# Performance work log

Measured on AMD Instinct MI355X. Metric: run time of the kernel, lower is better.

The kernel has to match this reference:

```python
import jax, jax.numpy as jnp
import numpy as np

N_SRC, N_DST, E = 10000, 10000, 640000
S, T, O, H = 128, 128, 128, 4
D = O // H


def setup_inputs() -> dict:
    key = jax.random.key(0)
    ks = jax.random.split(key, 12)
    f = lambda k, shape, fan: jax.random.normal(k, shape, dtype=jnp.float32) / np.float32(np.sqrt(fan))
    return {
        "x_src": jax.random.normal(ks[0], (N_SRC, S), dtype=jnp.float32),
        "x_dst": jax.random.normal(ks[1], (N_DST, T), dtype=jnp.float32),
        "W_pred1": f(ks[2], (S, T), T),
        "b_pred1": jnp.zeros((S,), jnp.float32),
        "W_pred2": f(ks[3], (S, S), S),
        "b_pred2": jnp.zeros((S,), jnp.float32),
        "W_res": f(ks[4], (H * D, S), S),
        "W_src": f(ks[5], (H * D, S), S),
        "W_dst": f(ks[6], (H * D, T), T),
        "att_src": jax.random.normal(ks[7], (1, H, D), dtype=jnp.float32) * 0.01,
        "att_dst": jax.random.normal(ks[8], (1, H, D), dtype=jnp.float32) * 0.01,
        "W_self": f(ks[9], (H * D, T), T),
        "b_self": jnp.zeros((H * D,), jnp.float32),
        "edge_src": jax.random.randint(ks[10], (E,), 0, N_SRC),
        "edge_dst": jax.random.randint(ks[11], (E,), 0, N_DST),
        "num_dst": N_DST,
    }


def reference(x_src, x_dst, W_pred1, b_pred1, W_pred2, b_pred2, W_res, W_src, W_dst,
              att_src, att_dst, W_self, b_self, edge_src, edge_dst, num_dst):
    h, d = att_src.shape[1], att_src.shape[2]
    # residual prediction path: pred_mlp(x_dst) = Lin2(ReLU(Lin1(x_dst)))
    pred = jax.nn.relu(x_dst @ W_pred1.T + b_pred1) @ W_pred2.T + b_pred2  # [Ndst,S]
    residual = x_src[edge_src] - pred[edge_dst]                            # [E,S]
    # per-node attention logits (equivalent to gather-then-dot, cheaper)
    a_s = ((x_src @ W_src.T).reshape(-1, h, d) * att_src).sum(-1)          # [Nsrc,H]
    a_d = ((x_dst @ W_dst.T).reshape(-1, h, d) * att_dst).sum(-1)          # [Ndst,H]
    alpha = jax.nn.leaky_relu(a_s[edge_src] + a_d[edge_dst], 0.2)          # [E,H]
    # edge softmax over incoming edges of each destination node
    amax = jax.ops.segment_max(alpha, edge_dst, num_segments=num_dst)      # [Ndst,H]
    ex = jnp.exp(alpha - amax[edge_dst])
    denom = jax.ops.segment_sum(ex, edge_dst, num_segments=num_dst)
    alpha = ex / (denom[edge_dst] + 1e-16)                                 # [E,H]
    # attention-weighted aggregation of transformed residuals
    msg = (residual @ W_res.T).reshape(-1, h, d) * alpha[:, :, None]       # [E,H,D]
    agg = jax.ops.segment_sum(msg.reshape(-1, h * d), edge_dst, num_segments=num_dst)
    return agg + x_dst @ W_self.T + b_self                                 # [Ndst,H*D]
```

## Files before the change

kernel.cpp:

```cpp
#include <hip/hip_runtime.h>

#define LEAKY 0.2f
#define CAP 160
#define CAPB 8192
#define CHUNK 2048
#define GSTRIDE 32

#define FMA4(A, S, V) do { (A).x += (S)*(V).x; (A).y += (S)*(V).y; (A).z += (S)*(V).z; (A).w += (S)*(V).w; } while (0)

struct GemmJob { const float* X; const float* W; const float* B; float* Y; int M; int relu; int bf16out; };

__device__ __forceinline__ unsigned short f2bf(float f) {
  unsigned int u = __float_as_uint(f);
  u += 0x7FFFu + ((u >> 16) & 1u);
  return (unsigned short)(u >> 16);
}
__device__ __forceinline__ float bf2f(unsigned short h) {
  return __uint_as_float(((unsigned int)h) << 16);
}

__device__ __forceinline__ void gemm128_block(
    const float* __restrict__ X, const float* __restrict__ W,
    const float* __restrict__ B, float* __restrict__ Y,
    int M, int relu, int bf16out, int row0,
    float* __restrict__ XsT , float* __restrict__ WTs ) {
  if (row0 >= M) return;
  const int tid = threadIdx.x;
  const int tx = tid & 15;
  const int ty = tid >> 4;
  float4 acc[8][2];
#pragma unroll
  for (int i = 0; i < 8; i++) {
    acc[i][0] = make_float4(0.f, 0.f, 0.f, 0.f);
    acc[i][1] = make_float4(0.f, 0.f, 0.f, 0.f);
  }
  const int rS = tid >> 1;
  const int kb = (tid & 1) * 8;

  for (int k0 = 0; k0 < 128; k0 += 16) {
    int rr = row0 + rS; if (rr >= M) rr = M - 1;
    const float* xp = X + (size_t)rr * 128 + k0 + kb;
    float4 a0 = *(const float4*)xp;
    float4 a1 = *(const float4*)(xp + 4);
    XsT[(kb + 0) * 128 + rS] = a0.x; XsT[(kb + 1) * 128 + rS] = a0.y;
    XsT[(kb + 2) * 128 + rS] = a0.z; XsT[(kb + 3) * 128 + rS] = a0.w;
    XsT[(kb + 4) * 128 + rS] = a1.x; XsT[(kb + 5) * 128 + rS] = a1.y;
    XsT[(kb + 6) * 128 + rS] = a1.z; XsT[(kb + 7) * 128 + rS] = a1.w;

    const float* wp = W + (size_t)rS * 128 + k0 + kb;
    float4 b0 = *(const float4*)wp;
    float4 b1 = *(const float4*)(wp + 4);
    WTs[(kb + 0) * 128 + rS] = b0.x; WTs[(kb + 1) * 128 + rS] = b0.y;
    WTs[(kb + 2) * 128 + rS] = b0.z; WTs[(kb + 3) * 128 + rS] = b0.w;
    WTs[(kb + 4) * 128 + rS] = b1.x; WTs[(kb + 5) * 128 + rS] = b1.y;
    WTs[(kb + 6) * 128 + rS] = b1.z; WTs[(kb + 7) * 128 + rS] = b1.w;
    __syncthreads();

#pragma unroll
    for (int k = 0; k < 16; k++) {
      float4 xa = *(const float4*)&XsT[k * 128 + ty * 4];
      float4 xb = *(const float4*)&XsT[k * 128 + 64 + ty * 4];
      float4 w0 = *(const float4*)&WTs[k * 128 + tx * 4];
      float4 w1 = *(const float4*)&WTs[k * 128 + 64 + tx * 4];
      FMA4(acc[0][0], xa.x, w0); FMA4(acc[0][1], xa.x, w1);
      FMA4(acc[1][0], xa.y, w0); FMA4(acc[1][1], xa.y, w1);
      FMA4(acc[2][0], xa.z, w0); FMA4(acc[2][1], xa.z, w1);
      FMA4(acc[3][0], xa.w, w0); FMA4(acc[3][1], xa.w, w1);
      FMA4(acc[4][0], xb.x, w0); FMA4(acc[4][1], xb.x, w1);
      FMA4(acc[5][0], xb.y, w0); FMA4(acc[5][1], xb.y, w1);
      FMA4(acc[6][0], xb.z, w0); FMA4(acc[6][1], xb.z, w1);
      FMA4(acc[7][0], xb.w, w0); FMA4(acc[7][1], xb.w, w1);
    }
    __syncthreads();
  }

  float4 bv0 = make_float4(0.f, 0.f, 0.f, 0.f);
  float4 bv1 = make_float4(0.f, 0.f, 0.f, 0.f);
  if (B) { bv0 = *(const float4*)(B + tx * 4); bv1 = *(const float4*)(B + 64 + tx * 4); }
#pragma unroll
  for (int i = 0; i < 8; i++) {
    int r = row0 + (i < 4 ? ty * 4 + i : 64 + ty * 4 + (i - 4));
    if (r < M) {
      float4 o0, o1;
      o0.x = acc[i][0].x + bv0.x; o0.y = acc[i][0].y + bv0.y;
      o0.z = acc[i][0].z + bv0.z; o0.w = acc[i][0].w + bv0.w;
      o1.x = acc[i][1].x + bv1.x; o1.y = acc[i][1].y + bv1.y;
      o1.z = acc[i][1].z + bv1.z; o1.w = acc[i][1].w + bv1.w;
      if (relu) {
        o0.x = fmaxf(o0.x, 0.f); o0.y = fmaxf(o0.y, 0.f);
        o0.z = fmaxf(o0.z, 0.f); o0.w = fmaxf(o0.w, 0.f);
        o1.x = fmaxf(o1.x, 0.f); o1.y = fmaxf(o1.y, 0.f);
        o1.z = fmaxf(o1.z, 0.f); o1.w = fmaxf(o1.w, 0.f);
      }
      if (bf16out) {
        unsigned short* yb = (unsigned short*)Y;
        ushort4 p0, p1;
        p0.x = f2bf(o0.x); p0.y = f2bf(o0.y); p0.z = f2bf(o0.z); p0.w = f2bf(o0.w);
        p1.x = f2bf(o1.x); p1.y = f2bf(o1.y); p1.z = f2bf(o1.z); p1.w = f2bf(o1.w);
        *(ushort4*)(yb + (size_t)r * 128 + tx * 4) = p0;
        *(ushort4*)(yb + (size_t)r * 128 + 64 + tx * 4) = p1;
      } else {
        *(float4*)(Y + (size_t)r * 128 + tx * 4) = o0;
        *(float4*)(Y + (size_t)r * 128 + 64 + tx * 4) = o1;
      }
    }
  }
}

__device__ __forceinline__ void attn32_block(const float* __restrict__ X,
                                             const float* __restrict__ v,
                                             float* __restrict__ a, int M, int blk,
                                             float* __restrict__ vsf ) {
  int tid = threadIdx.x;
  for (int i = tid; i < 512; i += 256) vsf[i + ((i >> 5) << 2)] = v[i];
  __syncthreads();
  int g = tid >> 3, l = tid & 7;
  int n = blk * 32 + g;
  if (n >= M) return;
  const float* xp = X + (size_t)n * 128 + l * 16;
  float4 x0 = *(const float4*)xp;
  float4 x1 = *(const float4*)(xp + 4);
  float4 x2 = *(const float4*)(xp + 8);
  float4 x3 = *(const float4*)(xp + 12);
  const float4* vv = (const float4*)vsf;
  int s = l * 18;
  float4 p = make_float4(0.f, 0.f, 0.f, 0.f);
  FMA4(p, x0.x, vv[s + 0]); FMA4(p, x0.y, vv[s + 1]); FMA4(p, x0.z, vv[s + 2]); FMA4(p, x0.w, vv[s + 3]);
  FMA4(p, x1.x, vv[s + 4]); FMA4(p, x1.y, vv[s + 5]); FMA4(p, x1.z, vv[s + 6]); FMA4(p, x1.w, vv[s + 7]);
  FMA4(p, x2.x, vv[s + 9]); FMA4(p, x2.y, vv[s +10]); FMA4(p, x2.z, vv[s +11]); FMA4(p, x2.w, vv[s +12]);
  FMA4(p, x3.x, vv[s +13]); FMA4(p, x3.y, vv[s +14]); FMA4(p, x3.z, vv[s +15]); FMA4(p, x3.w, vv[s +16]);
#pragma unroll
  for (int off = 1; off < 8; off <<= 1) {
    p.x += __shfl_xor(p.x, off, 64);
    p.y += __shfl_xor(p.y, off, 64);
    p.z += __shfl_xor(p.z, off, 64);
    p.w += __shfl_xor(p.w, off, 64);
  }
  if (l == 0) *(float4*)(a + (size_t)n * 4) = p;
}

__global__ __launch_bounds__(256) void phase1(
    const float* __restrict__ Wsrc, const float* __restrict__ attsrc,
    const float* __restrict__ Wdst, const float* __restrict__ attdst,
    const float* __restrict__ W_res, const float* __restrict__ W2,
    const float* __restrict__ b2,
    GemmJob jA,
    float* __restrict__ v_src, float* __restrict__ v_dst,
    float* __restrict__ Wc, float* __restrict__ bc,
    const int* __restrict__ edge_src, const int* __restrict__ edge_dst,
    int* __restrict__ gcnt, int* __restrict__ bin,
    int E, int Nd, int NB, int GA, int Q1, int T1) {
  __shared__ float smem[4096];
  int bx = blockIdx.x, tid = threadIdx.x;
  int u = (bx & 7) * Q1 + (bx >> 3);
  if (u >= T1) return;
  if (u == 0) {
    int which = tid >> 7, k = tid & 127;
    const float* W = which ? Wdst : Wsrc;
    const float* att = which ? attdst : attsrc;
    float* v = which ? v_dst : v_src;
    float s[4] = {0.f, 0.f, 0.f, 0.f};
#pragma unroll
    for (int h = 0; h < 4; h++)
      for (int d = 0; d < 32; d++)
        s[h] += W[(size_t)(h * 32 + d) * 128 + k] * att[h * 32 + d];
#pragma unroll
    for (int h = 0; h < 4; h++) v[k * 4 + h] = s[h];
  } else if (u == 1) {
    if (tid < 128) {
      float s = 0.f;
      for (int i = 0; i < 128; i++) s += W_res[(size_t)tid * 128 + i] * b2[i];
      bc[tid] = s;
    }
  } else if (u < 66) {
    int id = (u - 2) * 256 + tid;
    int o = id >> 7, j = id & 127;
    float s = 0.f;
    for (int i = 0; i < 128; i++) s += W_res[(size_t)o * 128 + i] * W2[(size_t)i * 128 + j];
    Wc[(size_t)o * 128 + j] = s;
  } else if (u < 66 + GA) {
    gemm128_block(jA.X, jA.W, jA.B, jA.Y, jA.M, jA.relu, jA.bf16out,
                  (u - 66) * 128, smem, smem + 2048);
  } else {
    int* pk    = (int*)smem;
    int* hist  = (int*)smem + CHUNK;
    int* gbase = hist + 160;
    int* lcur  = gbase + 160;
    int e0 = (u - 66 - GA) * CHUNK;
    int n = E - e0; if (n > CHUNK) n = CHUNK;
    if (n <= 0) return;
    for (int i = tid; i < NB; i += 256) hist[i] = 0;
    __syncthreads();
    for (int i = tid; i < n; i += 256) {
      int s = edge_src[e0 + i], d = edge_dst[e0 + i];
      pk[i] = (s << 14) | d;
      atomicAdd(&hist[d >> 6], 1);
    }
    __syncthreads();
    for (int b = tid; b < NB; b += 256) {
      gbase[b] = hist[b] ? atomicAdd(&gcnt[b * GSTRIDE], hist[b]) : 0;
      lcur[b] = 0;
    }
    __syncthreads();
    for (int i = tid; i < n; i += 256) {
      int p = pk[i];
      int b = (p & 16383) >> 6;
      int off = gbase[b] + atomicAdd(&lcur[b], 1);
      if (off < CAPB) bin[(size_t)b * CAPB + off] = p;
    }
  }
}

__global__ __launch_bounds__(256) void phase2(
    GemmJob j0, GemmJob j1, GemmJob j2,
    const float* __restrict__ x_src, const float* __restrict__ x_dst,
    const float* __restrict__ v_src, const float* __restrict__ v_dst,
    float* __restrict__ a_s, float* __restrict__ a_d,
    const int* __restrict__ gcnt, const int* __restrict__ bin,
    int* __restrict__ sorted_src, int* __restrict__ rstart, int* __restrict__ rend,
    int Ns, int Nd, int NB, int G, int As, int Ad, int Q2, int T2) {
  __shared__ float smem[4096];
  int bx = blockIdx.x, tid = threadIdx.x;
  int u = (bx % 6) * Q2 + bx / 6;
  if (u >= T2) return;
  if (u < 3 * G) {
    GemmJob J = (u < G) ? j0 : (u < 2 * G) ? j1 : j2;
    gemm128_block(J.X, J.W, J.B, J.Y, J.M, J.relu, J.bf16out, (u % G) * 128, smem, smem + 2048);
  } else if (u < 3 * G + As) {
    attn32_block(x_src, v_src, a_s, Ns, u - 3 * G, smem);
  } else if (u < 3 * G + As + Ad) {
    attn32_block(x_dst, v_dst, a_d, Nd, u - 3 * G - As, smem);
  } else {
    int b = u - (3 * G + As + Ad);
    int* hist2 = (int*)smem;
    int* lcur2 = (int*)smem + 64;
    int cnt = gcnt[b * GSTRIDE]; if (cnt > CAPB) cnt = CAPB;
    size_t base = (size_t)b * CAPB;
    if (tid < 64) hist2[tid] = 0;
    __syncthreads();
    for (int i = tid; i < cnt; i += 256) atomicAdd(&hist2[bin[base + i] & 63], 1);
    __syncthreads();
    if (tid < 64) {
      int v = hist2[tid];
      int incl = v;
#pragma unroll
      for (int off = 1; off < 64; off <<= 1) {
        int t = __shfl_up(incl, off, 64);
        if (tid >= off) incl += t;
      }
      int st = incl - v;
      lcur2[tid] = st;
      int dst = (b << 6) + tid;
      if (dst < Nd) {
        rstart[dst] = (int)base + st;
        rend[dst]   = (int)base + st + v;
      }
    }
    __syncthreads();
    for (int i = tid; i < cnt; i += 256) {
      int p = bin[base + i];
      int j = p & 63;
      int lp = atomicAdd(&lcur2[j], 1);
      sorted_src[base + lp] = p >> 14;
    }
  }
}

__global__ __launch_bounds__(256) void phase3(
    const int* __restrict__ rstart, const int* __restrict__ rend,
    const int* __restrict__ sorted_src,
    const float* __restrict__ a_s, const float* __restrict__ a_d,
    const unsigned short* __restrict__ u_src, const float* __restrict__ u_pred,
    const float* __restrict__ self_o, float* __restrict__ out, int Nd) {
  __shared__ float smem[1920];
  int bx = blockIdx.x, tid = threadIdx.x;
  int half = tid >> 7;
  int t = tid & 127;
  int dst = bx * 2 + half;
  if (dst >= Nd) return;

  float* wbuf  = smem + half * 640;
  int* srcbuf  = (int*)(smem + 1280) + half * 160;
  float4* red4 = (float4*)(smem + 1600);
  float4* redv = (float4*)(smem + 1616) + half * 32;
  float* inv_s = smem + 1872 + half * 4;
  float* sA_s  = smem + 1880 + half * 4;

  int start = rstart[dst];
  int deg = rend[dst] - start;
  float4 ad4 = *(const float4*)(a_d + (size_t)dst * 4);
  float s0 = 0.f, s1 = 0.f, s2 = 0.f, s3 = 0.f;
  for (int i = t; i < deg; i += 128) {
    int src = sorted_src[start + i];
    float4 as4 = *(const float4*)(a_s + (size_t)src * 4);
    float l0 = as4.x + ad4.x; l0 = l0 > 0.f ? l0 : LEAKY * l0;
    float l1 = as4.y + ad4.y; l1 = l1 > 0.f ? l1 : LEAKY * l1;
    float l2 = as4.z + ad4.z; l2 = l2 > 0.f ? l2 : LEAKY * l2;
    float l3 = as4.w + ad4.w; l3 = l3 > 0.f ? l3 : LEAKY * l3;
    float w0 = __expf(l0), w1 = __expf(l1), w2 = __expf(l2), w3 = __expf(l3);
    if (i < CAP) {
      wbuf[i * 4 + 0] = w0; wbuf[i * 4 + 1] = w1;
      wbuf[i * 4 + 2] = w2; wbuf[i * 4 + 3] = w3;
      srcbuf[i] = src;
    }
    s0 += w0; s1 += w1; s2 += w2; s3 += w3;
  }
  int wave = tid >> 6;
#pragma unroll
  for (int off = 32; off > 0; off >>= 1) {
    s0 += __shfl_xor(s0, off, 64);
    s1 += __shfl_xor(s1, off, 64);
    s2 += __shfl_xor(s2, off, 64);
    s3 += __shfl_xor(s3, off, 64);
  }
  if ((tid & 63) == 0) red4[wave] = make_float4(s0, s1, s2, s3);
  __syncthreads();
  if (t == 0) {
    float4 A = red4[half * 2], B = red4[half * 2 + 1];
    float dx = A.x + B.x, dy = A.y + B.y, dz = A.z + B.z, dw = A.w + B.w;
    inv_s[0] = 1.f / (dx + 1e-16f); sA_s[0] = dx * inv_s[0];
    inv_s[1] = 1.f / (dy + 1e-16f); sA_s[1] = dy * inv_s[1];
    inv_s[2] = 1.f / (dz + 1e-16f); sA_s[2] = dz * inv_s[2];
    inv_s[3] = 1.f / (dw + 1e-16f); sA_s[3] = dw * inv_s[3];
  }
  __syncthreads();

  int c4 = t & 31, rgrp = t >> 5, h = c4 >> 3;
  int coff = c4 * 4;
  float4 acc0 = make_float4(0.f,0.f,0.f,0.f), acc1 = acc0, acc2 = acc0, acc3 = acc0;
  int cap = deg < CAP ? deg : CAP;
  int i = rgrp;
  for (; i + 12 < cap; i += 16) {
    int sA = srcbuf[i], sB = srcbuf[i + 4], sC = srcbuf[i + 8], sD = srcbuf[i + 12];
    float wA = wbuf[i * 4 + h], wB = wbuf[(i + 4) * 4 + h];
    float wC = wbuf[(i + 8) * 4 + h], wD = wbuf[(i + 12) * 4 + h];
    ushort4 hA = *(const ushort4*)(u_src + (size_t)sA * 128 + coff);
    ushort4 hB = *(const ushort4*)(u_src + (size_t)sB * 128 + coff);
    ushort4 hC = *(const ushort4*)(u_src + (size_t)sC * 128 + coff);
    ushort4 hD = *(const ushort4*)(u_src + (size_t)sD * 128 + coff);
    float4 uA = make_float4(bf2f(hA.x), bf2f(hA.y), bf2f(hA.z), bf2f(hA.w));
    float4 uB = make_float4(bf2f(hB.x), bf2f(hB.y), bf2f(hB.z), bf2f(hB.w));
    float4 uC = make_float4(bf2f(hC.x), bf2f(hC.y), bf2f(hC.z), bf2f(hC.w));
    float4 uD = make_float4(bf2f(hD.x), bf2f(hD.y), bf2f(hD.z), bf2f(hD.w));
    FMA4(acc0, wA, uA); FMA4(acc1, wB, uB); FMA4(acc2, wC, uC); FMA4(acc3, wD, uD);
  }
  for (; i < cap; i += 4) {
    int s_ = srcbuf[i];
    float w = wbuf[i * 4 + h];
    ushort4 hh = *(const ushort4*)(u_src + (size_t)s_ * 128 + coff);
    float4 uu = make_float4(bf2f(hh.x), bf2f(hh.y), bf2f(hh.z), bf2f(hh.w));
    FMA4(acc0, w, uu);
  }
  if (deg > CAP) {
    float adh = (h == 0) ? ad4.x : (h == 1) ? ad4.y : (h == 2) ? ad4.z : ad4.w;
    for (int k = CAP + rgrp; k < deg; k += 4) {
      int src = sorted_src[start + k];
      float l = a_s[(size_t)src * 4 + h] + adh;
      l = l > 0.f ? l : LEAKY * l;
      float w = __expf(l);
      ushort4 hh = *(const ushort4*)(u_src + (size_t)src * 128 + coff);
      float4 uu = make_float4(bf2f(hh.x), bf2f(hh.y), bf2f(hh.z), bf2f(hh.w));
      FMA4(acc0, w, uu);
    }
  }
  float4 acc;
  acc.x = acc0.x + acc1.x + acc2.x + acc3.x;
  acc.y = acc0.y + acc1.y + acc2.y + acc3.y;
  acc.z = acc0.z + acc1.z + acc2.z + acc3.z;
  acc.w = acc0.w + acc1.w + acc2.w + acc3.w;
  acc.x += __shfl_xor(acc.x, 32, 64);
  acc.y += __shfl_xor(acc.y, 32, 64);
  acc.z += __shfl_xor(acc.z, 32, 64);
  acc.w += __shfl_xor(acc.w, 32, 64);
  if (t >= 64 && t < 96) redv[c4] = acc;
  __syncthreads();
  if (t < 32) {
    float4 r = redv[c4];
    acc.x += r.x; acc.y += r.y; acc.z += r.z; acc.w += r.w;
    float4 up = *(const float4*)(u_pred + (size_t)dst * 128 + coff);
    float4 so = *(const float4*)(self_o + (size_t)dst * 128 + coff);
    float iv = inv_s[h], sa = sA_s[h];
    float4 o;
    o.x = acc.x * iv - sa * up.x + so.x;
    o.y = acc.y * iv - sa * up.y + so.y;
    o.z = acc.z * iv - sa * up.z + so.z;
    o.w = acc.w * iv - sa * up.w + so.w;
    *(float4*)(out + (size_t)dst * 128 + coff) = o;
  }
}

extern "C" void kernel_launch(void* const* d_in, const int* in_sizes, int n_in,
                              void* d_out, int out_size, void* d_ws, size_t ws_size,
                              hipStream_t stream) {
  const float* x_src   = (const float*)d_in[0];
  const float* x_dst   = (const float*)d_in[1];
  const float* W_pred1 = (const float*)d_in[2];
  const float* b_pred1 = (const float*)d_in[3];
  const float* W_pred2 = (const float*)d_in[4];
  const float* b_pred2 = (const float*)d_in[5];
  const float* W_res   = (const float*)d_in[6];
  const float* W_src   = (const float*)d_in[7];
  const float* W_dst   = (const float*)d_in[8];
  const float* att_src = (const float*)d_in[9];
  const float* att_dst = (const float*)d_in[10];
  const float* W_self  = (const float*)d_in[11];
  const float* b_self  = (const float*)d_in[12];
  const int* edge_src  = (const int*)d_in[13];
  const int* edge_dst  = (const int*)d_in[14];
  int Ns = in_sizes[0] / 128;
  int Nd = in_sizes[1] / 128;
  int E  = in_sizes[13];
  float* out = (float*)d_out;
  int NB = (Nd + 63) >> 6;

  char* ws = (char*)d_ws;
  auto alloc = [&](size_t bytes) -> char* {
    char* p = ws;
    ws += (bytes + 255) & ~(size_t)255;
    return p;
  };
  float* relu1  = (float*)alloc((size_t)Nd * 128 * 4);
  unsigned short* u_src = (unsigned short*)alloc((size_t)Ns * 128 * 2);
  float* u_pred = (float*)alloc((size_t)Nd * 128 * 4);
  float* self_o = (float*)alloc((size_t)Nd * 128 * 4);
  float* a_s    = (float*)alloc((size_t)Ns * 4 * 4);
  float* a_d    = (float*)alloc((size_t)Nd * 4 * 4);
  float* v_src  = (float*)alloc(128 * 4 * 4);
  float* v_dst  = (float*)alloc(128 * 4 * 4);
  float* Wc     = (float*)alloc(128 * 128 * 4);
  float* bc     = (float*)alloc(128 * 4);
  int* gcnt     = (int*)alloc((size_t)NB * GSTRIDE * 4);
  int* rstart   = (int*)alloc((size_t)Nd * 4);
  int* rend     = (int*)alloc((size_t)Nd * 4);
  int* bin      = (int*)alloc((size_t)NB * CAPB * 4);
  int* sorted_src = (int*)alloc((size_t)NB * CAPB * 4);

  hipMemsetAsync(gcnt, 0, (size_t)NB * GSTRIDE * sizeof(int), stream);

  int GA  = (Nd + 127) / 128;
  int NCH = (E + CHUNK - 1) / CHUNK;
  int T1 = 66 + GA + NCH;
  int Q1 = (T1 + 7) / 8;
  GemmJob jA{ x_dst, W_pred1, b_pred1, relu1, Nd, 1, 0 };
  hipLaunchKernelGGL(phase1, dim3(Q1 * 8), dim3(256), 0, stream,
                     W_src, att_src, W_dst, att_dst, W_res, W_pred2, b_pred2, jA,
                     v_src, v_dst, Wc, bc, edge_src, edge_dst, gcnt, bin,
                     E, Nd, NB, GA, Q1, T1);

  int maxM = Ns > Nd ? Ns : Nd;
  int G  = (maxM + 127) / 128;
  int As = (Ns + 31) / 32;
  int Ad = (Nd + 31) / 32;
  int T2 = 3 * G + As + Ad + NB;
  int Q2 = (T2 + 5) / 6;
  GemmJob jB{ x_src, W_res,  nullptr, (float*)u_src, Ns, 0, 1 };
  GemmJob jC{ x_dst, W_self, b_self,  self_o, Nd, 0, 0 };
  GemmJob jU{ relu1, Wc,     bc,      u_pred, Nd, 0, 0 };
  hipLaunchKernelGGL(phase2, dim3(Q2 * 6), dim3(256), 0, stream,
                     jB, jC, jU, x_src, x_dst, v_src, v_dst, a_s, a_d,
                     gcnt, bin, sorted_src, rstart, rend,
                     Ns, Nd, NB, G, As, Ad, Q2, T2);

  hipLaunchKernelGGL(phase3, dim3((Nd + 1) / 2), dim3(256), 0, stream,
                     rstart, rend, sorted_src, a_s, a_d, u_src, u_pred, self_o, out, Nd);
}
```

Baseline: 166.5 us.

## Rebalance phases and fuse softmax denominator into single-pass aggregation

```diff
diff --git a/kernel.cpp b/kernel.cpp
--- a/kernel.cpp
+++ b/kernel.cpp
@@ -1,7 +1,6 @@
 #include <hip/hip_runtime.h>
 
 #define LEAKY 0.2f
-#define CAP 160
 #define CAPB 8192
 #define CHUNK 2048
 #define GSTRIDE 32
@@ -107,12 +106,24 @@
   }
 }
 
-__device__ __forceinline__ void attn32_block(const float* __restrict__ X,
-                                             const float* __restrict__ v,
-                                             float* __restrict__ a, int M, int blk,
-                                             float* __restrict__ vsf ) {
+__device__ __forceinline__ void attn32v_block(const float* __restrict__ X,
+                                              const float* __restrict__ W,
+                                              const float* __restrict__ att,
+                                              float* __restrict__ a, int M, int blk,
+                                              float* __restrict__ vsf ) {
   int tid = threadIdx.x;
-  for (int i = tid; i < 512; i += 256) vsf[i + ((i >> 5) << 2)] = v[i];
+  {
+    int k = tid & 127, hh = tid >> 7;
+#pragma unroll
+    for (int p = 0; p < 2; p++) {
+      int h = hh + p * 2;
+      float s = 0.f;
+      for (int d = 0; d < 32; d++)
+        s += W[(size_t)(h * 32 + d) * 128 + k] * att[h * 32 + d];
+      int i = k * 4 + h;
+      vsf[i + ((i >> 5) << 2)] = s;
+    }
+  }
   __syncthreads();
   int g = tid >> 3, l = tid & 7;
   int n = blk * 32 + g;
@@ -144,49 +155,60 @@
     const float* __restrict__ Wdst, const float* __restrict__ attdst,
     const float* __restrict__ W_res, const float* __restrict__ W2,
     const float* __restrict__ b2,
-    GemmJob jA,
-    float* __restrict__ v_src, float* __restrict__ v_dst,
+    GemmJob jA, GemmJob jB, GemmJob jC,
+    const float* __restrict__ x_src, const float* __restrict__ x_dst,
+    float* __restrict__ a_s, float* __restrict__ a_d,
     float* __restrict__ Wc, float* __restrict__ bc,
     const int* __restrict__ edge_src, const int* __restrict__ edge_dst,
     int* __restrict__ gcnt, int* __restrict__ bin,
-    int E, int Nd, int NB, int GA, int Q1, int T1) {
+    int E, int Ns, int Nd, int NB,
+    int GA, int GB, int GC, int As, int Ad, int Q1, int T1) {
   __shared__ float smem[4096];
   int bx = blockIdx.x, tid = threadIdx.x;
   int u = (bx & 7) * Q1 + (bx >> 3);
   if (u >= T1) return;
   if (u == 0) {
-    int which = tid >> 7, k = tid & 127;
-    const float* W = which ? Wdst : Wsrc;
-    const float* att = which ? attdst : attsrc;
-    float* v = which ? v_dst : v_src;
-    float s[4] = {0.f, 0.f, 0.f, 0.f};
-#pragma unroll
-    for (int h = 0; h < 4; h++)
-      for (int d = 0; d < 32; d++)
-        s[h] += W[(size_t)(h * 32 + d) * 128 + k] * att[h * 32 + d];
-#pragma unroll
-    for (int h = 0; h < 4; h++) v[k * 4 + h] = s[h];
-  } else if (u == 1) {
     if (tid < 128) {
       float s = 0.f;
       for (int i = 0; i < 128; i++) s += W_res[(size_t)tid * 128 + i] * b2[i];
       bc[tid] = s;
     }
-  } else if (u < 66) {
-    int id = (u - 2) * 256 + tid;
+    return;
+  }
+  if (u < 65) {
+    int id = (u - 1) * 256 + tid;
     int o = id >> 7, j = id & 127;
     float s = 0.f;
     for (int i = 0; i < 128; i++) s += W_res[(size_t)o * 128 + i] * W2[(size_t)i * 128 + j];
     Wc[(size_t)o * 128 + j] = s;
-  } else if (u < 66 + GA) {
-    gemm128_block(jA.X, jA.W, jA.B, jA.Y, jA.M, jA.relu, jA.bf16out,
-                  (u - 66) * 128, smem, smem + 2048);
-  } else {
+    return;
+  }
+  int r = u - 65;
+  if (r < GA) {
+    gemm128_block(jA.X, jA.W, jA.B, jA.Y, jA.M, jA.relu, jA.bf16out, r * 128, smem, smem + 2048);
+    return;
+  }
+  r -= GA;
+  if (r < GB) {
+    gemm128_block(jB.X, jB.W, jB.B, jB.Y, jB.M, jB.relu, jB.bf16out, r * 128, smem, smem + 2048);
+    return;
+  }
+  r -= GB;
+  if (r < GC) {
+    gemm128_block(jC.X, jC.W, jC.B, jC.Y, jC.M, jC.relu, jC.bf16out, r * 128, smem, smem + 2048);
+    return;
+  }
+  r -= GC;
+  if (r < As) { attn32v_block(x_src, Wsrc, attsrc, a_s, Ns, r, smem); return; }
+  r -= As;
+  if (r < Ad) { attn32v_block(x_dst, Wdst, attdst, a_d, Nd, r, smem); return; }
+  r -= Ad;
+  {
     int* pk    = (int*)smem;
     int* hist  = (int*)smem + CHUNK;
     int* gbase = hist + 160;
     int* lcur  = gbase + 160;
-    int e0 = (u - 66 - GA) * CHUNK;
+    int e0 = r * CHUNK;
     int n = E - e0; if (n > CHUNK) n = CHUNK;
     if (n <= 0) return;
     for (int i = tid; i < NB; i += 256) hist[i] = 0;
@@ -212,57 +234,49 @@
 }
 
 __global__ __launch_bounds__(256) void phase2(
-    GemmJob j0, GemmJob j1, GemmJob j2,
-    const float* __restrict__ x_src, const float* __restrict__ x_dst,
-    const float* __restrict__ v_src, const float* __restrict__ v_dst,
-    float* __restrict__ a_s, float* __restrict__ a_d,
+    GemmJob jU,
     const int* __restrict__ gcnt, const int* __restrict__ bin,
     int* __restrict__ sorted_src, int* __restrict__ rstart, int* __restrict__ rend,
-    int Ns, int Nd, int NB, int G, int As, int Ad, int Q2, int T2) {
+    int Nd, int NB, int GU, int Q2, int T2) {
   __shared__ float smem[4096];
   int bx = blockIdx.x, tid = threadIdx.x;
-  int u = (bx % 6) * Q2 + bx / 6;
+  int u = (bx % 3) * Q2 + bx / 3;
   if (u >= T2) return;
-  if (u < 3 * G) {
-    GemmJob J = (u < G) ? j0 : (u < 2 * G) ? j1 : j2;
-    gemm128_block(J.X, J.W, J.B, J.Y, J.M, J.relu, J.bf16out, (u % G) * 128, smem, smem + 2048);
-  } else if (u < 3 * G + As) {
-    attn32_block(x_src, v_src, a_s, Ns, u - 3 * G, smem);
-  } else if (u < 3 * G + As + Ad) {
-    attn32_block(x_dst, v_dst, a_d, Nd, u - 3 * G - As, smem);
-  } else {
-    int b = u - (3 * G + As + Ad);
-    int* hist2 = (int*)smem;
-    int* lcur2 = (int*)smem + 64;
-    int cnt = gcnt[b * GSTRIDE]; if (cnt > CAPB) cnt = CAPB;
-    size_t base = (size_t)b * CAPB;
-    if (tid < 64) hist2[tid] = 0;
-    __syncthreads();
-    for (int i = tid; i < cnt; i += 256) atomicAdd(&hist2[bin[base + i] & 63], 1);
-    __syncthreads();
-    if (tid < 64) {
-      int v = hist2[tid];
-      int incl = v;
-#pragma unroll
-      for (int off = 1; off < 64; off <<= 1) {
-        int t = __shfl_up(incl, off, 64);
-        if (tid >= off) incl += t;
-      }
-      int st = incl - v;
-      lcur2[tid] = st;
-      int dst = (b << 6) + tid;
-      if (dst < Nd) {
-        rstart[dst] = (int)base + st;
-        rend[dst]   = (int)base + st + v;
-      }
-    }
-    __syncthreads();
-    for (int i = tid; i < cnt; i += 256) {
-      int p = bin[base + i];
-      int j = p & 63;
-      int lp = atomicAdd(&lcur2[j], 1);
-      sorted_src[base + lp] = p >> 14;
-    }
+  if (u < GU) {
+    gemm128_block(jU.X, jU.W, jU.B, jU.Y, jU.M, jU.relu, jU.bf16out, u * 128, smem, smem + 2048);
+    return;
+  }
+  int b = u - GU;
+  int* hist2 = (int*)smem;
+  int* lcur2 = (int*)smem + 64;
+  int cnt = gcnt[b * GSTRIDE]; if (cnt > CAPB) cnt = CAPB;
+  size_t base = (size_t)b * CAPB;
+  if (tid < 64) hist2[tid] = 0;
+  __syncthreads();
+  for (int i = tid; i < cnt; i += 256) atomicAdd(&hist2[bin[base + i] & 63], 1);
+  __syncthreads();
+  if (tid < 64) {
+    int v = hist2[tid];
+    int incl = v;
+#pragma unroll
+    for (int off = 1; off < 64; off <<= 1) {
+      int t = __shfl_up(incl, off, 64);
+      if (tid >= off) incl += t;
+    }
+    int st = incl - v;
+    lcur2[tid] = st;
+    int dst = (b << 6) + tid;
+    if (dst < Nd) {
+      rstart[dst] = (int)base + st;
+      rend[dst]   = (int)base + st + v;
+    }
+  }
+  __syncthreads();
+  for (int i = tid; i < cnt; i += 256) {
+    int p = bin[base + i];
+    int j = p & 63;
+    int lp = atomicAdd(&lcur2[j], 1);
+    sorted_src[base + lp] = p >> 14;
   }
 }
 
@@ -272,119 +286,76 @@
     const float* __restrict__ a_s, const float* __restrict__ a_d,
     const unsigned short* __restrict__ u_src, const float* __restrict__ u_pred,
     const float* __restrict__ self_o, float* __restrict__ out, int Nd) {
-  __shared__ float smem[1920];
+  __shared__ float4 redv[64];
+  __shared__ float  rdn[64];
   int bx = blockIdx.x, tid = threadIdx.x;
-  int half = tid >> 7;
-  int t = tid & 127;
+  int half = tid >> 7, t = tid & 127;
   int dst = bx * 2 + half;
   if (dst >= Nd) return;
-
-  float* wbuf  = smem + half * 640;
-  int* srcbuf  = (int*)(smem + 1280) + half * 160;
-  float4* red4 = (float4*)(smem + 1600);
-  float4* redv = (float4*)(smem + 1616) + half * 32;
-  float* inv_s = smem + 1872 + half * 4;
-  float* sA_s  = smem + 1880 + half * 4;
-
   int start = rstart[dst];
   int deg = rend[dst] - start;
-  float4 ad4 = *(const float4*)(a_d + (size_t)dst * 4);
-  float s0 = 0.f, s1 = 0.f, s2 = 0.f, s3 = 0.f;
-  for (int i = t; i < deg; i += 128) {
-    int src = sorted_src[start + i];
-    float4 as4 = *(const float4*)(a_s + (size_t)src * 4);
-    float l0 = as4.x + ad4.x; l0 = l0 > 0.f ? l0 : LEAKY * l0;
-    float l1 = as4.y + ad4.y; l1 = l1 > 0.f ? l1 : LEAKY * l1;
-    float l2 = as4.z + ad4.z; l2 = l2 > 0.f ? l2 : LEAKY * l2;
-    float l3 = as4.w + ad4.w; l3 = l3 > 0.f ? l3 : LEAKY * l3;
-    float w0 = __expf(l0), w1 = __expf(l1), w2 = __expf(l2), w3 = __expf(l3);
-    if (i < CAP) {
-      wbuf[i * 4 + 0] = w0; wbuf[i * 4 + 1] = w1;
-      wbuf[i * 4 + 2] = w2; wbuf[i * 4 + 3] = w3;
-      srcbuf[i] = src;
-    }
-    s0 += w0; s1 += w1; s2 += w2; s3 += w3;
-  }
-  int wave = tid >> 6;
-#pragma unroll
-  for (int off = 32; off > 0; off >>= 1) {
-    s0 += __shfl_xor(s0, off, 64);
-    s1 += __shfl_xor(s1, off, 64);
-    s2 += __shfl_xor(s2, off, 64);
-    s3 += __shfl_xor(s3, off, 64);
-  }
-  if ((tid & 63) == 0) red4[wave] = make_float4(s0, s1, s2, s3);
-  __syncthreads();
-  if (t == 0) {
-    float4 A = red4[half * 2], B = red4[half * 2 + 1];
-    float dx = A.x + B.x, dy = A.y + B.y, dz = A.z + B.z, dw = A.w + B.w;
-    inv_s[0] = 1.f / (dx + 1e-16f); sA_s[0] = dx * inv_s[0];
-    inv_s[1] = 1.f / (dy + 1e-16f); sA_s[1] = dy * inv_s[1];
-    inv_s[2] = 1.f / (dz + 1e-16f); sA_s[2] = dz * inv_s[2];
-    inv_s[3] = 1.f / (dw + 1e-16f); sA_s[3] = dw * inv_s[3];
-  }
-  __syncthreads();
-
-  int c4 = t & 31, rgrp = t >> 5, h = c4 >> 3;
-  int coff = c4 * 4;
-  float4 acc0 = make_float4(0.f,0.f,0.f,0.f), acc1 = acc0, acc2 = acc0, acc3 = acc0;
-  int cap = deg < CAP ? deg : CAP;
+  int c4 = t & 31, rgrp = t >> 5, h = c4 >> 3, coff = c4 * 4;
+  float adh = a_d[(size_t)dst * 4 + h];
+
+  float4 acc[8];
+  float dnm[4] = {0.f, 0.f, 0.f, 0.f};
+#pragma unroll
+  for (int j = 0; j < 8; j++) acc[j] = make_float4(0.f, 0.f, 0.f, 0.f);
+
   int i = rgrp;
-  for (; i + 12 < cap; i += 16) {
-    int sA = srcbuf[i], sB = srcbuf[i + 4], sC = srcbuf[i + 8], sD = srcbuf[i + 12];
-    float wA = wbuf[i * 4 + h], wB = wbuf[(i + 4) * 4 + h];
-    float wC = wbuf[(i + 8) * 4 + h], wD = wbuf[(i + 12) * 4 + h];
-    ushort4 hA = *(const ushort4*)(u_src + (size_t)sA * 128 + coff);
-    ushort4 hB = *(const ushort4*)(u_src + (size_t)sB * 128 + coff);
-    ushort4 hC = *(const ushort4*)(u_src + (size_t)sC * 128 + coff);
-    ushort4 hD = *(const ushort4*)(u_src + (size_t)sD * 128 + coff);
-    float4 uA = make_float4(bf2f(hA.x), bf2f(hA.y), bf2f(hA.z), bf2f(hA.w));
-    float4 uB = make_float4(bf2f(hB.x), bf2f(hB.y), bf2f(hB.z), bf2f(hB.w));
-    float4 uC = make_float4(bf2f(hC.x), bf2f(hC.y), bf2f(hC.z), bf2f(hC.w));
-    float4 uD = make_float4(bf2f(hD.x), bf2f(hD.y), bf2f(hD.z), bf2f(hD.w));
-    FMA4(acc0, wA, uA); FMA4(acc1, wB, uB); FMA4(acc2, wC, uC); FMA4(acc3, wD, uD);
-  }
-  for (; i < cap; i += 4) {
-    int s_ = srcbuf[i];
-    float w = wbuf[i * 4 + h];
-    ushort4 hh = *(const ushort4*)(u_src + (size_t)s_ * 128 + coff);
-    float4 uu = make_float4(bf2f(hh.x), bf2f(hh.y), bf2f(hh.z), bf2f(hh.w));
-    FMA4(acc0, w, uu);
-  }
-  if (deg > CAP) {
-    float adh = (h == 0) ? ad4.x : (h == 1) ? ad4.y : (h == 2) ? ad4.z : ad4.w;
-    for (int k = CAP + rgrp; k < deg; k += 4) {
-      int src = sorted_src[start + k];
+  for (; i + 28 < deg; i += 32) {
+#pragma unroll
+    for (int j = 0; j < 8; j++) {
+      int src = sorted_src[start + i + j * 4];
       float l = a_s[(size_t)src * 4 + h] + adh;
       l = l > 0.f ? l : LEAKY * l;
       float w = __expf(l);
-      ushort4 hh = *(const ushort4*)(u_src + (size_t)src * 128 + coff);
-      float4 uu = make_float4(bf2f(hh.x), bf2f(hh.y), bf2f(hh.z), bf2f(hh.w));
-      FMA4(acc0, w, uu);
-    }
-  }
-  float4 acc;
-  acc.x = acc0.x + acc1.x + acc2.x + acc3.x;
-  acc.y = acc0.y + acc1.y + acc2.y + acc3.y;
-  acc.z = acc0.z + acc1.z + acc2.z + acc3.z;
-  acc.w = acc0.w + acc1.w + acc2.w + acc3.w;
-  acc.x += __shfl_xor(acc.x, 32, 64);
-  acc.y += __shfl_xor(acc.y, 32, 64);
-  acc.z += __shfl_xor(acc.z, 32, 64);
-  acc.w += __shfl_xor(acc.w, 32, 64);
-  if (t >= 64 && t < 96) redv[c4] = acc;
+      dnm[j & 3] += w;
+      ushort4 hh4 = *(const ushort4*)(u_src + (size_t)src * 128 + coff);
+      acc[j].x += w * bf2f(hh4.x);
+      acc[j].y += w * bf2f(hh4.y);
+      acc[j].z += w * bf2f(hh4.z);
+      acc[j].w += w * bf2f(hh4.w);
+    }
+  }
+  for (; i < deg; i += 4) {
+    int src = sorted_src[start + i];
+    float l = a_s[(size_t)src * 4 + h] + adh;
+    l = l > 0.f ? l : LEAKY * l;
+    float w = __expf(l);
+    dnm[0] += w;
+    ushort4 hh4 = *(const ushort4*)(u_src + (size_t)src * 128 + coff);
+    acc[0].x += w * bf2f(hh4.x);
+    acc[0].y += w * bf2f(hh4.y);
+    acc[0].z += w * bf2f(hh4.z);
+    acc[0].w += w * bf2f(hh4.w);
+  }
+  float4 A;
+  A.x = ((acc[0].x + acc[1].x) + (acc[2].x + acc[3].x)) + ((acc[4].x + acc[5].x) + (acc[6].x + acc[7].x));
+  A.y = ((acc[0].y + acc[1].y) + (acc[2].y + acc[3].y)) + ((acc[4].y + acc[5].y) + (acc[6].y + acc[7].y));
+  A.z = ((acc[0].z + acc[1].z) + (acc[2].z + acc[3].z)) + ((acc[4].z + acc[5].z) + (acc[6].z + acc[7].z));
+  A.w = ((acc[0].w + acc[1].w) + (acc[2].w + acc[3].w)) + ((acc[4].w + acc[5].w) + (acc[6].w + acc[7].w));
+  float D = (dnm[0] + dnm[1]) + (dnm[2] + dnm[3]);
+  A.x += __shfl_xor(A.x, 32, 64);
+  A.y += __shfl_xor(A.y, 32, 64);
+  A.z += __shfl_xor(A.z, 32, 64);
+  A.w += __shfl_xor(A.w, 32, 64);
+  D   += __shfl_xor(D,   32, 64);
+  if (t >= 64 && t < 96) { redv[half * 32 + c4] = A; rdn[half * 32 + c4] = D; }
   __syncthreads();
   if (t < 32) {
-    float4 r = redv[c4];
-    acc.x += r.x; acc.y += r.y; acc.z += r.z; acc.w += r.w;
+    float4 rr = redv[half * 32 + c4];
+    A.x += rr.x; A.y += rr.y; A.z += rr.z; A.w += rr.w;
+    D += rdn[half * 32 + c4];
+    float inv = 1.f / (D + 1e-16f);
+    float sa = D * inv;
     float4 up = *(const float4*)(u_pred + (size_t)dst * 128 + coff);
     float4 so = *(const float4*)(self_o + (size_t)dst * 128 + coff);
-    float iv = inv_s[h], sa = sA_s[h];
     float4 o;
-    o.x = acc.x * iv - sa * up.x + so.x;
-    o.y = acc.y * iv - sa * up.y + so.y;
-    o.z = acc.z * iv - sa * up.z + so.z;
-    o.w = acc.w * iv - sa * up.w + so.w;
+    o.x = A.x * inv - sa * up.x + so.x;
+    o.y = A.y * inv - sa * up.y + so.y;
+    o.z = A.z * inv - sa * up.z + so.z;
+    o.w = A.w * inv - sa * up.w + so.w;
     *(float4*)(out + (size_t)dst * 128 + coff) = o;
   }
 }
@@ -425,8 +396,6 @@
   float* self_o = (float*)alloc((size_t)Nd * 128 * 4);
   float* a_s    = (float*)alloc((size_t)Ns * 4 * 4);
   float* a_d    = (float*)alloc((size_t)Nd * 4 * 4);
-  float* v_src  = (float*)alloc(128 * 4 * 4);
-  float* v_dst  = (float*)alloc(128 * 4 * 4);
   float* Wc     = (float*)alloc(128 * 128 * 4);
   float* bc     = (float*)alloc(128 * 4);
   int* gcnt     = (int*)alloc((size_t)NB * GSTRIDE * 4);
@@ -438,28 +407,28 @@
   hipMemsetAsync(gcnt, 0, (size_t)NB * GSTRIDE * sizeof(int), stream);
 
   int GA  = (Nd + 127) / 128;
+  int GB  = (Ns + 127) / 128;
+  int GC  = (Nd + 127) / 128;
+  int As  = (Ns + 31) / 32;
+  int Ad  = (Nd + 31) / 32;
   int NCH = (E + CHUNK - 1) / CHUNK;
-  int T1 = 66 + GA + NCH;
+  int T1 = 65 + GA + GB + GC + As + Ad + NCH;
   int Q1 = (T1 + 7) / 8;
   GemmJob jA{ x_dst, W_pred1, b_pred1, relu1, Nd, 1, 0 };
-  hipLaunchKernelGGL(phase1, dim3(Q1 * 8), dim3(256), 0, stream,
-                     W_src, att_src, W_dst, att_dst, W_res, W_pred2, b_pred2, jA,
-                     v_src, v_dst, Wc, bc, edge_src, edge_dst, gcnt, bin,
-                     E, Nd, NB, GA, Q1, T1);
-
-  int maxM = Ns > Nd ? Ns : Nd;
-  int G  = (maxM + 127) / 128;
-  int As = (Ns + 31) / 32;
-  int Ad = (Nd + 31) / 32;
-  int T2 = 3 * G + As + Ad + NB;
-  int Q2 = (T2 + 5) / 6;
   GemmJob jB{ x_src, W_res,  nullptr, (float*)u_src, Ns, 0, 1 };
   GemmJob jC{ x_dst, W_self, b_self,  self_o, Nd, 0, 0 };
-  GemmJob jU{ relu1, Wc,     bc,      u_pred, Nd, 0, 0 };
-  hipLaunchKernelGGL(phase2, dim3(Q2 * 6), dim3(256), 0, stream,
-                     jB, jC, jU, x_src, x_dst, v_src, v_dst, a_s, a_d,
-                     gcnt, bin, sorted_src, rstart, rend,
-                     Ns, Nd, NB, G, As, Ad, Q2, T2);
+  hipLaunchKernelGGL(phase1, dim3(Q1 * 8), dim3(256), 0, stream,
+                     W_src, att_src, W_dst, att_dst, W_res, W_pred2, b_pred2,
+                     jA, jB, jC, x_src, x_dst, a_s, a_d, Wc, bc,
+                     edge_src, edge_dst, gcnt, bin,
+                     E, Ns, Nd, NB, GA, GB, GC, As, Ad, Q1, T1);
+
+  GemmJob jU{ relu1, Wc, bc, u_pred, Nd, 0, 0 };
+  int GU = (Nd + 127) / 128;
+  int T2 = GU + NB;
+  int Q2 = (T2 + 2) / 3;
+  hipLaunchKernelGGL(phase2, dim3(Q2 * 3), dim3(256), 0, stream,
+                     jU, gcnt, bin, sorted_src, rstart, rend, Nd, NB, GU, Q2, T2);
 
   hipLaunchKernelGGL(phase3, dim3((Nd + 1) / 2), dim3(256), 0, stream,
                      rstart, rend, sorted_src, a_s, a_d, u_src, u_pred, self_o, out, Nd);
```

Result: slower. 201.1 us (+20.8%).
